# Optimization experiments

Measured on AMD Instinct MI355X. Metric: run time of the kernel, lower is better.

The kernel has to match this reference:

```python
import jax, jax.numpy as jnp
import numpy as np
from jax import lax

BITS = 8
STRIDE = 1
PADDING = 1
SCALE = 2.0 ** (BITS - 1)  # fixed-point scale 2^(bits-1)


def setup_inputs() -> dict:
    key = jax.random.key(0)
    k1, k2, k3 = jax.random.split(key, 3)
    x = jax.random.normal(k1, (32, 128, 56, 56), dtype=jnp.float32)
    W = jax.random.normal(k2, (256, 128, 3, 3), dtype=jnp.float32)
    b = jax.random.normal(k3, (256,), dtype=jnp.float32)
    return {"x": x, "W": W, "b": b}


def reference(x, W, b):
    # to_fix_point: round(v * 2^(bits-1)); torch keeps long ints, but all
    # arithmetic in forward promotes back to float, so float round is exact here.
    w_q = jnp.round(W * SCALE)
    b_q = jnp.round(b * SCALE)
    # calConv: out[i,j] = sum(patch * w_q) / 2^(bits-1) + b_q
    # (square 3x3 kernel makes the original's transposed patch indexing a standard conv)
    out = lax.conv_general_dilated(
        x, w_q,
        window_strides=(STRIDE, STRIDE),
        padding=[(PADDING, PADDING), (PADDING, PADDING)],
        dimension_numbers=("NCHW", "OIHW", "NCHW"),
    )
    return out / SCALE + b_q[None, :, None, None]
```

## Files before the change

kernel.cpp:

```cpp
#include <hip/hip_runtime.h>

typedef _Float16 half8 __attribute__((ext_vector_type(8)));
typedef float floatx4 __attribute__((ext_vector_type(4)));

#define IMG   3136
#define PIMG  3364
#define XP_ELEMS (32 * 58 * 58 * 128)
#define WQ_ELEMS (9 * 256 * 128)

#define AS1 __attribute__((address_space(1)))
#define AS3 __attribute__((address_space(3)))

__global__ __launch_bounds__(256) void prep_kernel(const float* __restrict__ x,
                                                   const float* __restrict__ W,
                                                   _Float16* __restrict__ xp,
                                                   _Float16* __restrict__ wq) {
    const int bid = blockIdx.x;
    const int t   = threadIdx.x;
    if (bid >= 1856) {
        int U = (bid - 1856) * 256 + t;
        int l  = U & 63;
        int wv = (U >> 6) & 7;
        int g  = (U >> 9) & 1;
        int h  = (U >> 10) & 1;
        int T  = U >> 11;
        int rs = T >> 1, kt = T & 1;
        int k  = h * 128 + g * 64 + wv * 8 + (l >> 3);
        int c0 = kt * 64 + (((l & 7) ^ ((l >> 3) & 7)) * 8);
        _Float16* d = wq + (long)U * 8;
        #pragma unroll
        for (int j = 0; j < 8; ++j)
            d[j] = (_Float16)rintf(W[(k * 128 + c0 + j) * 9 + rs] * 128.0f);
        return;
    }
    const int hh = bid % 58;
    const int n  = bid / 58;
    _Float16* rowbase = xp + ((long)(n * 58 + hh) * 58) * 128;

    if (hh == 0 || hh == 57) {
        #pragma unroll
        for (int i = 0; i < 4; ++i) {
            int idx = i * 256 + t;
            if (idx < 928) *(half8*)(rowbase + idx * 8) = (half8)(_Float16)0.0f;
        }
        return;
    }

    __shared__ _Float16 tile[128 * 57];
    const int h = hh - 1;

    #pragma unroll
    for (int p = 0; p < 7; ++p) {
        int idx = p * 256 + t;
        int c   = idx / 14;
        int w4  = (idx % 14) * 4;
        const float4 v = *(const float4*)(x + ((long)(n * 128 + c) * 56 + h) * 56 + w4);
        _Float16* d = tile + c * 57 + w4;
        d[0] = (_Float16)v.x; d[1] = (_Float16)v.y;
        d[2] = (_Float16)v.z; d[3] = (_Float16)v.w;
    }
    __syncthreads();

    #pragma unroll
    for (int p = 0; p < 4; ++p) {
        int idx = p * 256 + t;
        if (idx < 896) {
            int ww = idx >> 4;
            int c0 = (idx & 15) * 8;
            half8 v;
            #pragma unroll
            for (int j = 0; j < 8; ++j) v[j] = tile[(c0 + j) * 57 + ww];
            *(half8*)(rowbase + (ww + 1) * 128 + c0) = v;
        }
    }
    if (t < 32) {
        int ww = (t >> 4) ? 57 : 0;
        int c0 = (t & 15) * 8;
        *(half8*)(rowbase + ww * 128 + c0) = (half8)(_Float16)0.0f;
    }
}

__global__ __launch_bounds__(512, 2) void conv_mfma_kernel(
    const _Float16* __restrict__ xp, const _Float16* __restrict__ wq,
    const float* __restrict__ b, float* __restrict__ out)
{
    __shared__ __align__(16) _Float16 smem[65536];

    const int tid = threadIdx.x;
    const int l   = tid & 63;
    const int wv  = tid >> 6;
    const int wm  = wv & 1;
    const int wn  = wv >> 1;
    int bx  = blockIdx.x;
    bx = (bx & 7) * 49 + (bx >> 3);

    const int lr3  = l >> 3;
    const int l7   = l & 7;
    const int l47  = l >> 4;
    const int lswz = ((l & 7) ^ (lr3 & 7)) * 16;

    long pbB[4];
    #pragma unroll
    for (int hg = 0; hg < 4; ++hg) {
        const int pix = bx * 256 + hg * 64 + wv * 8 + lr3;
        const int n = pix / IMG, hw = pix % IMG;
        pbB[hg] = (long)(n * PIMG + (hw / 56) * 58 + (hw % 56)) * 256 + lswz;
    }
    const long abase = (long)wv * 1024 + l * 16;

    floatx4 acc[8][4] = {};

    auto stageA = [&](int T, int h, int pbuf) {
        const char* src = (const char*)wq + (long)((T * 2 + h) * 2) * 8192 + abase;
        _Float16* dst = smem + pbuf * 32768 + (h * 128 + wv * 8) * 64;
        __builtin_amdgcn_global_load_lds((AS1 void*)src,          (AS3 void*)dst,          16, 0, 0);
        __builtin_amdgcn_global_load_lds((AS1 void*)(src + 8192), (AS3 void*)(dst + 4096), 16, 0, 0);
    };
    auto stageB = [&](int T, int h, int pbuf) {
        const int rs = T >> 1, kt = T & 1;
        const int r  = (rs * 11) >> 5;
        const int s2 = rs - r * 3;
        const long toff = (long)(r * 58 + s2) * 256 + kt * 128;
        const char* xb = (const char*)xp + toff;
        _Float16* dst = smem + pbuf * 32768 + 16384 + (h * 128 + wv * 8) * 64;
        __builtin_amdgcn_global_load_lds((AS1 void*)(xb + pbB[h * 2 + 0]), (AS3 void*)dst,          16, 0, 0);
        __builtin_amdgcn_global_load_lds((AS1 void*)(xb + pbB[h * 2 + 1]), (AS3 void*)(dst + 4096), 16, 0, 0);
    };

    const int arow = wm * 128 + (l & 15);
    const int brow = wn * 64 + (l & 15);

    #define QUAD(q) { \
        __builtin_amdgcn_s_setprio(1); \
        _Pragma("unroll") for (int i = 0; i < 2; ++i) { \
            const int mi = (q) * 2 + i; \
            const half8 af0 = *(const half8*)(As + (arow + mi * 16) * 64 + ((0 + l47) ^ l7) * 8); \
            const half8 af1 = *(const half8*)(As + (arow + mi * 16) * 64 + ((4 + l47) ^ l7) * 8); \
            _Pragma("unroll") for (int ni = 0; ni < 4; ++ni) { \
                acc[mi][ni] = __builtin_amdgcn_mfma_f32_16x16x32_f16(af0, bf[ni][0], acc[mi][ni], 0, 0, 0); \
                acc[mi][ni] = __builtin_amdgcn_mfma_f32_16x16x32_f16(af1, bf[ni][1], acc[mi][ni], 0, 0, 0); \
            } \
        } \
        __builtin_amdgcn_s_setprio(0); \
    }

    stageA(0, 0, 0); stageA(0, 1, 0); stageB(0, 0, 0); stageB(0, 1, 0);

    #pragma unroll 2
    for (int T = 0; T < 18; ++T) {
        const int pb = T & 1;
        const _Float16* As = smem + pb * 32768;
        const _Float16* Bs = As + 16384;
        asm volatile("s_barrier" ::: "memory");
        if (T < 17) {
            stageA(T + 1, 0, pb ^ 1);
            asm volatile("s_waitcnt vmcnt(2)" ::: "memory");
        } else {
            asm volatile("s_waitcnt vmcnt(0)" ::: "memory");
        }
        asm volatile("s_barrier" ::: "memory");
        half8 bf[4][2];
        #pragma unroll
        for (int ni = 0; ni < 4; ++ni) {
            bf[ni][0] = *(const half8*)(Bs + (brow + ni * 16) * 64 + ((0 + l47) ^ l7) * 8);
            bf[ni][1] = *(const half8*)(Bs + (brow + ni * 16) * 64 + ((4 + l47) ^ l7) * 8);
        }
        QUAD(0)
        if (T < 17) stageA(T + 1, 1, pb ^ 1);
        QUAD(1)
        if (T < 17) stageB(T + 1, 0, pb ^ 1);
        QUAD(2)
        if (T < 17) stageB(T + 1, 1, pb ^ 1);
        QUAD(3)
    }
    #undef QUAD

    #pragma unroll
    for (int mi = 0; mi < 8; ++mi) {
        const int kb = wm * 128 + mi * 16 + (l >> 4) * 4;
        #pragma unroll
        for (int rg = 0; rg < 4; ++rg) {
            const int k = kb + rg;
            const float bq = rintf(b[k] * 128.0f);
            #pragma unroll
            for (int ni = 0; ni < 4; ++ni) {
                const int pix = bx * 256 + wn * 64 + ni * 16 + (l & 15);
                const int n  = pix / IMG;
                const int pr = pix - n * IMG;
                out[((long)n * 256 + k) * IMG + pr] = acc[mi][ni][rg] * (1.0f / 128.0f) + bq;
            }
        }
    }
}

__global__ void conv_fallback_kernel(const float* __restrict__ x, const float* __restrict__ W,
                                     const float* __restrict__ b, float* __restrict__ out)
{
    __shared__ float wsm[1152];
    const int k = blockIdx.y;
    for (int i = threadIdx.x; i < 1152; i += 256)
        wsm[i] = rintf(W[k * 1152 + i] * 128.0f);
    __syncthreads();
    const int pix = blockIdx.x * 256 + threadIdx.x;
    const int n = pix / IMG, hw = pix % IMG;
    const int h = hw / 56, w = hw % 56;
    float acc = 0.0f;
    for (int c = 0; c < 128; ++c) {
        const float* xr = x + ((n * 128 + c) * 56) * 56;
        const float* wr = wsm + c * 9;
        #pragma unroll
        for (int r = 0; r < 3; ++r) {
            const int hh = h + r - 1;
            if ((unsigned)hh >= 56u) continue;
            #pragma unroll
            for (int s = 0; s < 3; ++s) {
                const int ww = w + s - 1;
                if ((unsigned)ww >= 56u) continue;
                acc += xr[hh * 56 + ww] * wr[r * 3 + s];
            }
        }
    }
    out[((long)n * 256 + k) * IMG + hw] = acc * (1.0f / 128.0f) + rintf(b[k] * 128.0f);
}

extern "C" void kernel_launch(void* const* d_in, const int* in_sizes, int n_in,
                              void* d_out, int out_size, void* d_ws, size_t ws_size,
                              hipStream_t stream) {
    const float* x = (const float*)d_in[0];
    const float* W = (const float*)d_in[1];
    const float* b = (const float*)d_in[2];
    float* out = (float*)d_out;

    const size_t need = (size_t)XP_ELEMS * 2 + (size_t)WQ_ELEMS * 2;
    if (ws_size >= need) {
        _Float16* xp = (_Float16*)d_ws;
        _Float16* wq = xp + XP_ELEMS;
        prep_kernel<<<2000, 256, 0, stream>>>(x, W, xp, wq);
        conv_mfma_kernel<<<dim3(392), 512, 0, stream>>>(xp, wq, b, out);
    } else {
        conv_fallback_kernel<<<dim3(392, 256), 256, 0, stream>>>(x, W, b, out);
    }
}
```

Baseline: 204.4 us.

## Restructure main loop into phased LDS-read/prefetch/MFMA schedule with per-phase barriers

Reorganizes each K-iteration into four phases. Each phase first issues its A-fragment LDS reads, then optionally issues the next tile's global->LDS prefetches, waits on lgkmcnt, and runs the MFMAs followed by a barrier. All prefetches are now issued in the first two phases, and the loop top waits vmcnt(0) instead of vmcnt(2). The aim is to pull LDS reads ahead of the MFMA clusters and keep waves in lockstep, at the cost of four extra barriers per iteration and an earlier full drain of outstanding global loads.

Measured after the change: 204.7 us. About the same (+0.2%).

```diff
diff --git a/kernel.cpp b/kernel.cpp
--- a/kernel.cpp
+++ b/kernel.cpp
@@ -130,18 +130,25 @@
     const int arow = wm * 128 + (l & 15);
     const int brow = wn * 64 + (l & 15);
 
-    #define QUAD(q) { \
+    #define PHASE(q, STAGE_STMT) { \
+        half8 af0[2], af1[2]; \
+        _Pragma("unroll") for (int i = 0; i < 2; ++i) { \
+            const int mi = (q) * 2 + i; \
+            af0[i] = *(const half8*)(As + (arow + mi * 16) * 64 + ((0 + l47) ^ l7) * 8); \
+            af1[i] = *(const half8*)(As + (arow + mi * 16) * 64 + ((4 + l47) ^ l7) * 8); \
+        } \
+        STAGE_STMT \
+        asm volatile("s_waitcnt lgkmcnt(0)" ::: "memory"); \
         __builtin_amdgcn_s_setprio(1); \
         _Pragma("unroll") for (int i = 0; i < 2; ++i) { \
             const int mi = (q) * 2 + i; \
-            const half8 af0 = *(const half8*)(As + (arow + mi * 16) * 64 + ((0 + l47) ^ l7) * 8); \
-            const half8 af1 = *(const half8*)(As + (arow + mi * 16) * 64 + ((4 + l47) ^ l7) * 8); \
             _Pragma("unroll") for (int ni = 0; ni < 4; ++ni) { \
-                acc[mi][ni] = __builtin_amdgcn_mfma_f32_16x16x32_f16(af0, bf[ni][0], acc[mi][ni], 0, 0, 0); \
-                acc[mi][ni] = __builtin_amdgcn_mfma_f32_16x16x32_f16(af1, bf[ni][1], acc[mi][ni], 0, 0, 0); \
+                acc[mi][ni] = __builtin_amdgcn_mfma_f32_16x16x32_f16(af0[i], bf[ni][0], acc[mi][ni], 0, 0, 0); \
+                acc[mi][ni] = __builtin_amdgcn_mfma_f32_16x16x32_f16(af1[i], bf[ni][1], acc[mi][ni], 0, 0, 0); \
             } \
         } \
         __builtin_amdgcn_s_setprio(0); \
+        asm volatile("s_barrier" ::: "memory"); \
     }
 
     stageA(0, 0, 0); stageA(0, 1, 0); stageB(0, 0, 0); stageB(0, 1, 0);
@@ -151,13 +158,7 @@
         const int pb = T & 1;
         const _Float16* As = smem + pb * 32768;
         const _Float16* Bs = As + 16384;
-        asm volatile("s_barrier" ::: "memory");
-        if (T < 17) {
-            stageA(T + 1, 0, pb ^ 1);
-            asm volatile("s_waitcnt vmcnt(2)" ::: "memory");
-        } else {
-            asm volatile("s_waitcnt vmcnt(0)" ::: "memory");
-        }
+        asm volatile("s_waitcnt vmcnt(0)" ::: "memory");
         asm volatile("s_barrier" ::: "memory");
         half8 bf[4][2];
         #pragma unroll
@@ -165,15 +166,12 @@
             bf[ni][0] = *(const half8*)(Bs + (brow + ni * 16) * 64 + ((0 + l47) ^ l7) * 8);
             bf[ni][1] = *(const half8*)(Bs + (brow + ni * 16) * 64 + ((4 + l47) ^ l7) * 8);
         }
-        QUAD(0)
-        if (T < 17) stageA(T + 1, 1, pb ^ 1);
-        QUAD(1)
-        if (T < 17) stageB(T + 1, 0, pb ^ 1);
-        QUAD(2)
-        if (T < 17) stageB(T + 1, 1, pb ^ 1);
-        QUAD(3)
-    }
-    #undef QUAD
+        PHASE(0, { if (T < 17) { stageA(T + 1, 0, pb ^ 1); stageA(T + 1, 1, pb ^ 1); } })
+        PHASE(1, { if (T < 17) { stageB(T + 1, 0, pb ^ 1); stageB(T + 1, 1, pb ^ 1); } })
+        PHASE(2, { })
+        PHASE(3, { })
+    }
+    #undef PHASE
 
     #pragma unroll
     for (int mi = 0; mi < 8; ++mi) {
```

## Swap MFMA operand roles for vectorized stores and restructure LDS prefetch schedule

Applied to the files above, without the earlier changes.

Swaps the MFMA operand roles so pixels become the M dimension and filters the N dimension. Each lane's four accumulator values are then contiguous pixels and can be written with a single float4 store instead of scalar strided stores. The main loop now loads all A and B fragments from LDS up front, issues the next tile's global-to-LDS prefetches, and runs one uninterrupted block of MFMAs. One barrier moves to the end of the iteration. This holds more fragments in registers (pf[8][2]) at 2 waves/SIMD occupancy, which raises register pressure and removes the interleaving of loads with compute.

Measured after the change: 208.5 us. +2.0%, slower.

```diff
diff --git a/kernel.cpp b/kernel.cpp
--- a/kernel.cpp
+++ b/kernel.cpp
@@ -89,8 +89,8 @@
     const int tid = threadIdx.x;
     const int l   = tid & 63;
     const int wv  = tid >> 6;
-    const int wm  = wv & 1;
-    const int wn  = wv >> 1;
+    const int wp  = wv & 1;
+    const int wf  = wv >> 1;
     int bx  = blockIdx.x;
     bx = (bx & 7) * 49 + (bx >> 3);
 
@@ -127,68 +127,66 @@
         __builtin_amdgcn_global_load_lds((AS1 void*)(xb + pbB[h * 2 + 1]), (AS3 void*)(dst + 4096), 16, 0, 0);
     };
 
-    const int arow = wm * 128 + (l & 15);
-    const int brow = wn * 64 + (l & 15);
-
-    #define QUAD(q) { \
-        __builtin_amdgcn_s_setprio(1); \
-        _Pragma("unroll") for (int i = 0; i < 2; ++i) { \
-            const int mi = (q) * 2 + i; \
-            const half8 af0 = *(const half8*)(As + (arow + mi * 16) * 64 + ((0 + l47) ^ l7) * 8); \
-            const half8 af1 = *(const half8*)(As + (arow + mi * 16) * 64 + ((4 + l47) ^ l7) * 8); \
-            _Pragma("unroll") for (int ni = 0; ni < 4; ++ni) { \
-                acc[mi][ni] = __builtin_amdgcn_mfma_f32_16x16x32_f16(af0, bf[ni][0], acc[mi][ni], 0, 0, 0); \
-                acc[mi][ni] = __builtin_amdgcn_mfma_f32_16x16x32_f16(af1, bf[ni][1], acc[mi][ni], 0, 0, 0); \
-            } \
-        } \
-        __builtin_amdgcn_s_setprio(0); \
-    }
-
-    stageA(0, 0, 0); stageA(0, 1, 0); stageB(0, 0, 0); stageB(0, 1, 0);
+    const int frow = wf * 64  + (l & 15);
+    const int prow = wp * 128 + (l & 15);
+
+    stageB(0, 0, 0); stageB(0, 1, 0); stageA(0, 0, 0); stageA(0, 1, 0);
 
     #pragma unroll 2
     for (int T = 0; T < 18; ++T) {
         const int pb = T & 1;
         const _Float16* As = smem + pb * 32768;
         const _Float16* Bs = As + 16384;
-        asm volatile("s_barrier" ::: "memory");
         if (T < 17) {
-            stageA(T + 1, 0, pb ^ 1);
+            stageB(T + 1, 0, pb ^ 1);
             asm volatile("s_waitcnt vmcnt(2)" ::: "memory");
         } else {
             asm volatile("s_waitcnt vmcnt(0)" ::: "memory");
         }
         asm volatile("s_barrier" ::: "memory");
-        half8 bf[4][2];
+
+        half8 ff[4][2], pf[8][2];
         #pragma unroll
         for (int ni = 0; ni < 4; ++ni) {
-            bf[ni][0] = *(const half8*)(Bs + (brow + ni * 16) * 64 + ((0 + l47) ^ l7) * 8);
-            bf[ni][1] = *(const half8*)(Bs + (brow + ni * 16) * 64 + ((4 + l47) ^ l7) * 8);
-        }
-        QUAD(0)
-        if (T < 17) stageA(T + 1, 1, pb ^ 1);
-        QUAD(1)
-        if (T < 17) stageB(T + 1, 0, pb ^ 1);
-        QUAD(2)
-        if (T < 17) stageB(T + 1, 1, pb ^ 1);
-        QUAD(3)
-    }
-    #undef QUAD
+            ff[ni][0] = *(const half8*)(As + (frow + ni * 16) * 64 + ((0 + l47) ^ l7) * 8);
+            ff[ni][1] = *(const half8*)(As + (frow + ni * 16) * 64 + ((4 + l47) ^ l7) * 8);
+        }
+        #pragma unroll
+        for (int mi = 0; mi < 8; ++mi) {
+            pf[mi][0] = *(const half8*)(Bs + (prow + mi * 16) * 64 + ((0 + l47) ^ l7) * 8);
+            pf[mi][1] = *(const half8*)(Bs + (prow + mi * 16) * 64 + ((4 + l47) ^ l7) * 8);
+        }
+        if (T < 17) { stageB(T + 1, 1, pb ^ 1); stageA(T + 1, 0, pb ^ 1); stageA(T + 1, 1, pb ^ 1); }
+
+        __builtin_amdgcn_s_setprio(1);
+        #pragma unroll
+        for (int kk = 0; kk < 2; ++kk)
+            #pragma unroll
+            for (int mi = 0; mi < 8; ++mi)
+                #pragma unroll
+                for (int ni = 0; ni < 4; ++ni)
+                    acc[mi][ni] = __builtin_amdgcn_mfma_f32_16x16x32_f16(pf[mi][kk], ff[ni][kk], acc[mi][ni], 0, 0, 0);
+        __builtin_amdgcn_s_setprio(0);
+
+        asm volatile("s_barrier" ::: "memory");
+    }
 
     #pragma unroll
     for (int mi = 0; mi < 8; ++mi) {
-        const int kb = wm * 128 + mi * 16 + (l >> 4) * 4;
-        #pragma unroll
-        for (int rg = 0; rg < 4; ++rg) {
-            const int k = kb + rg;
-            const float bq = rintf(b[k] * 128.0f);
-            #pragma unroll
-            for (int ni = 0; ni < 4; ++ni) {
-                const int pix = bx * 256 + wn * 64 + ni * 16 + (l & 15);
-                const int n  = pix / IMG;
-                const int pr = pix - n * IMG;
-                out[((long)n * 256 + k) * IMG + pr] = acc[mi][ni][rg] * (1.0f / 128.0f) + bq;
-            }
+        const int pix = bx * 256 + wp * 128 + mi * 16 + (l >> 4) * 4;
+        const int n  = pix / IMG;
+        const int pr = pix - n * IMG;
+        float* orow = out + (long)n * 256 * IMG + pr;
+        #pragma unroll
+        for (int ni = 0; ni < 4; ++ni) {
+            const int filt = wf * 64 + ni * 16 + (l & 15);
+            const float bq = rintf(b[filt] * 128.0f);
+            float4 v;
+            v.x = acc[mi][ni][0] * (1.0f / 128.0f) + bq;
+            v.y = acc[mi][ni][1] * (1.0f / 128.0f) + bq;
+            v.z = acc[mi][ni][2] * (1.0f / 128.0f) + bq;
+            v.w = acc[mi][ni][3] * (1.0f / 128.0f) + bq;
+            *(float4*)(orow + (long)filt * IMG) = v;
         }
     }
 }
```
